# Optimization experiments

Hardware: AMD Instinct MI355X
Metric: run time of the kernel (lower is better)

## Reference

```python
import jax, jax.numpy as jnp
import numpy as np

N_NODES = 50000
N_EDGES = 800000
D = 128
N_GRAPHS = 128
N_CLASSES = 10
BN_EPS = 1e-5


def setup_inputs() -> dict:
    key = jax.random.key(0)
    ks = jax.random.split(key, 8)
    x = jax.random.normal(ks[0], (N_NODES, D), dtype=jnp.float32)
    edge_index = jax.random.randint(ks[1], (2, N_EDGES), 0, N_NODES, dtype=jnp.int64)
    batch = jnp.sort(jax.random.randint(ks[2], (N_NODES,), 0, N_GRAPHS, dtype=jnp.int64))
    s = 1.0 / np.sqrt(D)
    W1a = jax.random.normal(ks[3], (D, D), dtype=jnp.float32) * s
    W1b = jax.random.normal(ks[4], (D, D), dtype=jnp.float32) * s
    W2a = jax.random.normal(ks[5], (D, D), dtype=jnp.float32) * s
    W2b = jax.random.normal(ks[6], (D, D), dtype=jnp.float32) * s
    Wo = jax.random.normal(ks[7], (D, N_CLASSES), dtype=jnp.float32) * s
    z = jnp.zeros((D,), jnp.float32)
    o = jnp.ones((D,), jnp.float32)
    return dict(x=x, edge_index=edge_index, batch=batch,
                W1a=W1a, b1a=z, W1b=W1b, b1b=z, g1=o, be1=z,
                W2a=W2a, b2a=z, W2b=W2b, b2b=z, g2=o, be2=z,
                Wo=Wo, bo=jnp.zeros((N_CLASSES,), jnp.float32))


def _gin_conv(x, edge_index, Wa, ba, Wb, bb):
    # message passing: gather source features, scatter-add to targets (eps=0)
    msgs = x[edge_index[0]]                                   # [E, D]
    agg = jax.ops.segment_sum(msgs, edge_index[1], num_segments=x.shape[0])
    h = agg + x                                               # (1+eps)*x + sum_j x_j
    h = jnp.maximum(h @ Wa + ba, 0.0)                         # Linear -> ReLU
    return h @ Wb + bb                                        # Linear


def _bn_relu(h, gamma, beta):
    # BatchNorm1d (training mode: batch stats, biased var) + ReLU
    mu = jnp.mean(h, axis=0)
    var = jnp.mean(jnp.square(h - mu), axis=0)
    hn = (h - mu) * jax.lax.rsqrt(var + BN_EPS) * gamma + beta
    return jnp.maximum(hn, 0.0)


def reference(x, edge_index, batch,
              W1a, b1a, W1b, b1b, g1, be1,
              W2a, b2a, W2b, b2b, g2, be2,
              Wo, bo):
    h = _gin_conv(x, edge_index, W1a, b1a, W1b, b1b)
    h = _bn_relu(h, g1, be1)
    h = _gin_conv(h, edge_index, W2a, b2a, W2b, b2b)
    h = _bn_relu(h, g2, be2)
    pooled = jax.ops.segment_sum(h, batch, num_segments=N_GRAPHS)  # global_add_pool
    return pooled @ Wo + bo
```

## Files before the change

### kernel.cpp

```cpp
#include <hip/hip_runtime.h>

typedef __attribute__((ext_vector_type(8))) short bf16x8;
typedef __attribute__((ext_vector_type(4))) float f32x4;
typedef __attribute__((ext_vector_type(2))) float f32x2;
typedef __attribute__((ext_vector_type(2))) unsigned u32x2;

#define N_NODES 50000
#define N_EDGES 800000
#define DIM 128
#define N_GRAPHS 128
#define N_CLASSES 10
#define BN_EPS 1e-5f
#define FBLK ((N_NODES + 63) / 64)
#define FGRID (FBLK / 2)
#define NPART (FBLK * 4)
#define RED_NB 64
#define RED_ROWS ((NPART + RED_NB - 1) / RED_NB)

#define NBUCK 196
#define FILL_NB 400
#define FILL_PER (N_EDGES / FILL_NB)
#define BMAX 6144

#define CVT_NB (N_NODES * 64 / 256)
#define PREPW_NB 256

static __device__ __forceinline__ unsigned short f2bf(float f) {
    unsigned u = __float_as_uint(f);
    u += 0x7FFF + ((u >> 16) & 1);
    return (unsigned short)(u >> 16);
}
static __device__ __forceinline__ float bf_lo(unsigned u) { return __uint_as_float(u << 16); }
static __device__ __forceinline__ float bf_hi(unsigned u) { return __uint_as_float(u & 0xffff0000u); }
static __device__ __forceinline__ unsigned packbf(float a, float b) {
    return (unsigned)f2bf(a) | ((unsigned)f2bf(b) << 16);
}

__global__ __launch_bounds__(256) void prep_all(const f32x2* __restrict__ x,
                                                unsigned* __restrict__ xb,
                                                const float* __restrict__ W0,
                                                const float* __restrict__ W1,
                                                const float* __restrict__ W2,
                                                const float* __restrict__ W3,
                                                unsigned short* __restrict__ wf,
                                                const int* __restrict__ batch,
                                                int* __restrict__ gs,
                                                const int* __restrict__ ei,
                                                int* __restrict__ gbcnt) {
    int b = blockIdx.x, tid = threadIdx.x;
    if (b < CVT_NB) {
        int t = b * 256 + tid;
        f32x2 v = x[t];
        xb[t] = packbf(v[0], v[1]);
    } else if (b < CVT_NB + PREPW_NB) {
        int t = (b - CVT_NB) * 256 + tid;
        int m = t >> 14, rem = t & 16383;
        int e = rem & 7, lane = (rem >> 3) & 63, fi = rem >> 9;
        int ks = fi & 3, n = fi >> 2;
        int col = n * 16 + (lane & 15);
        int k = ks * 32 + ((lane >> 4) << 3) + e;
        const float* W = (m == 0) ? W0 : (m == 1) ? W1 : (m == 2) ? W2 : W3;
        wf[t] = f2bf(W[k * DIM + col]);
    } else if (b < CVT_NB + PREPW_NB + FILL_NB) {
        __shared__ int cnt[NBUCK];
        if (tid < NBUCK) cnt[tid] = 0;
        __syncthreads();
        int e0 = (b - CVT_NB - PREPW_NB) * FILL_PER;
        for (int c = tid; c < FILL_PER; c += 256) {
            int dst = ei[N_EDGES + e0 + c];
            atomicAdd(&cnt[dst >> 8], 1);
        }
        __syncthreads();
        if (tid < NBUCK) atomicAdd(&gbcnt[tid], cnt[tid]);
    } else {
        int g = tid;
        if (g > N_GRAPHS) return;
        int lo = 0, hi = N_NODES;
        while (lo < hi) {
            int mid = (lo + hi) >> 1;
            if (batch[mid] < g) lo = mid + 1; else hi = mid;
        }
        gs[g] = lo;
    }
}

__global__ __launch_bounds__(256) void bucket_scan(const int* __restrict__ gbcnt,
                                                   int* __restrict__ boff,
                                                   int* __restrict__ gcur) {
    __shared__ int buf[256];
    int t = threadIdx.x;
    int v = (t < NBUCK) ? gbcnt[t] : 0;
    buf[t] = v;
    __syncthreads();
#pragma unroll
    for (int off = 1; off < 256; off <<= 1) {
        int u = (t >= off) ? buf[t - off] : 0;
        __syncthreads();
        buf[t] += u;
        __syncthreads();
    }
    if (t < NBUCK) { int ex = buf[t] - v; boff[t] = ex; gcur[t] = ex; }
    if (t == 0) boff[NBUCK] = N_EDGES;
}

__global__ __launch_bounds__(256) void bucket_fill(const int* __restrict__ ei,
                                                   int* __restrict__ gcur,
                                                   unsigned* __restrict__ gbuf) {
    __shared__ unsigned ent[FILL_PER];
    __shared__ unsigned srt[FILL_PER];
    __shared__ int cnt[256], c2[256], lofs[256], gbase[256];
    int tid = threadIdx.x;
    int e0 = blockIdx.x * FILL_PER;
    cnt[tid] = 0; c2[tid] = 0;
    __syncthreads();
    for (int i = tid; i < FILL_PER; i += 256) {
        int src = ei[e0 + i];
        int dst = ei[N_EDGES + e0 + i];
        ent[i] = (unsigned)src | ((unsigned)(dst & 255) << 16) | ((unsigned)(dst >> 8) << 24);
        atomicAdd(&cnt[dst >> 8], 1);
    }
    __syncthreads();
    int v = cnt[tid];
    lofs[tid] = v;
    __syncthreads();
#pragma unroll
    for (int off = 1; off < 256; off <<= 1) {
        int u = (tid >= off) ? lofs[tid - off] : 0;
        __syncthreads();
        lofs[tid] += u;
        __syncthreads();
    }
    int excl = lofs[tid] - v;
    lofs[tid] = excl;
    if (tid < NBUCK && v > 0) gbase[tid] = atomicAdd(&gcur[tid], v);
    __syncthreads();
    for (int i = tid; i < FILL_PER; i += 256) {
        unsigned w = ent[i];
        int b = w >> 24;
        int r = atomicAdd(&c2[b], 1);
        srt[lofs[b] + r] = w;
    }
    __syncthreads();
    for (int i = tid; i < FILL_PER; i += 256) {
        unsigned w = srt[i];
        int b = w >> 24;
        gbuf[gbase[b] + (i - lofs[b])] = w;
    }
}

__global__ __launch_bounds__(256) void csr_build(const unsigned* __restrict__ gbuf,
                                                 const int* __restrict__ boff,
                                                 unsigned short* __restrict__ csr16,
                                                 int* __restrict__ row_start) {
    __shared__ unsigned ent[BMAX];
    __shared__ unsigned short csl[BMAX];
    __shared__ int cnt[256], c2[256], offs[256];
    int b = blockIdx.x, t = threadIdx.x;
    int base = boff[b], n = boff[b + 1] - base;
    for (int i = t; i < n; i += 256) ent[i] = gbuf[base + i];
    cnt[t] = 0; c2[t] = 0;
    __syncthreads();
    for (int i = t; i < n; i += 256) atomicAdd(&cnt[(ent[i] >> 16) & 255], 1);
    __syncthreads();
    int v = cnt[t];
    offs[t] = v;
    __syncthreads();
#pragma unroll
    for (int off = 1; off < 256; off <<= 1) {
        int u = (t >= off) ? offs[t - off] : 0;
        __syncthreads();
        offs[t] += u;
        __syncthreads();
    }
    int excl = offs[t] - v;
    int node = b * 256 + t;
    if (node < N_NODES) row_start[node] = base + excl;
    if (b == NBUCK - 1 && t == 0) row_start[N_NODES] = N_EDGES;
    __syncthreads();
    offs[t] = excl;
    __syncthreads();
    for (int i = t; i < n; i += 256) {
        unsigned w = ent[i];
        int d = (w >> 16) & 255;
        int r = atomicAdd(&c2[d], 1);
        csl[offs[d] + r] = (unsigned short)(w & 0xffffu);
    }
    __syncthreads();
    for (int i = t; i < n; i += 256) csr16[base + i] = csl[i];
}

template <bool BN>
__global__ __launch_bounds__(256) void aggregate_bf(const u32x2* __restrict__ F2,
                                                    u32x2* __restrict__ out,
                                                    const int* __restrict__ row_start,
                                                    const unsigned short* __restrict__ csr16,
                                                    const float* __restrict__ scale,
                                                    const float* __restrict__ shift) {
    int wave = threadIdx.x >> 6, lane = threadIdx.x & 63;
    int v = blockIdx.x * 4 + wave;
    if (v >= N_NODES) return;
    int half = lane >> 5;
    int c4 = lane & 31;
    f32x4 sc, sh;
    if (BN) {
        sc = ((const f32x4*)scale)[c4];
        sh = ((const f32x4*)shift)[c4];
    }
    int e0 = row_start[v];
    int n = row_start[v + 1] - e0;
    int myidx = (lane < n) ? (int)csr16[e0 + lane] : 0;
    int n64 = (n < 64) ? n : 64;

    f32x4 a0 = f32x4{0.f, 0.f, 0.f, 0.f};
    f32x4 a1 = f32x4{0.f, 0.f, 0.f, 0.f};
    if (half == 0) {
        u32x2 u = F2[(size_t)v * 32 + c4];
        a0[0] = bf_lo(u[0]); a0[1] = bf_hi(u[0]);
        a0[2] = bf_lo(u[1]); a0[3] = bf_hi(u[1]);
        if (BN) {
#pragma unroll
            for (int k = 0; k < 4; ++k) a0[k] = fmaxf(a0[k] * sc[k] + sh[k], 0.f);
        }
    }

    for (int base = 0; base < n64; base += 8) {
        int j0 = base + half, j1 = j0 + 2, j2 = j0 + 4, j3 = j0 + 6;
        int s0 = __shfl(myidx, j0 & 63, 64);
        int s1 = __shfl(myidx, j1 & 63, 64);
        int s2 = __shfl(myidx, j2 & 63, 64);
        int s3 = __shfl(myidx, j3 & 63, 64);
        u32x2 ua = F2[(size_t)s0 * 32 + c4];
        u32x2 ub = F2[(size_t)s1 * 32 + c4];
        u32x2 uc = F2[(size_t)s2 * 32 + c4];
        u32x2 ud = F2[(size_t)s3 * 32 + c4];
        float p0 = bf_lo(ua[0]), p1 = bf_hi(ua[0]), p2 = bf_lo(ua[1]), p3 = bf_hi(ua[1]);
        float q0 = bf_lo(ub[0]), q1 = bf_hi(ub[0]), q2 = bf_lo(ub[1]), q3 = bf_hi(ub[1]);
        float r0 = bf_lo(uc[0]), r1 = bf_hi(uc[0]), r2 = bf_lo(uc[1]), r3 = bf_hi(uc[1]);
        float t0 = bf_lo(ud[0]), t1 = bf_hi(ud[0]), t2 = bf_lo(ud[1]), t3 = bf_hi(ud[1]);
        if (BN) {
            p0 = fmaxf(p0 * sc[0] + sh[0], 0.f); p1 = fmaxf(p1 * sc[1] + sh[1], 0.f);
            p2 = fmaxf(p2 * sc[2] + sh[2], 0.f); p3 = fmaxf(p3 * sc[3] + sh[3], 0.f);
            q0 = fmaxf(q0 * sc[0] + sh[0], 0.f); q1 = fmaxf(q1 * sc[1] + sh[1], 0.f);
            q2 = fmaxf(q2 * sc[2] + sh[2], 0.f); q3 = fmaxf(q3 * sc[3] + sh[3], 0.f);
            r0 = fmaxf(r0 * sc[0] + sh[0], 0.f); r1 = fmaxf(r1 * sc[1] + sh[1], 0.f);
            r2 = fmaxf(r2 * sc[2] + sh[2], 0.f); r3 = fmaxf(r3 * sc[3] + sh[3], 0.f);
            t0 = fmaxf(t0 * sc[0] + sh[0], 0.f); t1 = fmaxf(t1 * sc[1] + sh[1], 0.f);
            t2 = fmaxf(t2 * sc[2] + sh[2], 0.f); t3 = fmaxf(t3 * sc[3] + sh[3], 0.f);
        }
        if (j0 < n64) { a0[0] += p0; a0[1] += p1; a0[2] += p2; a0[3] += p3; }
        if (j1 < n64) { a0[0] += q0; a0[1] += q1; a0[2] += q2; a0[3] += q3; }
        if (j2 < n64) { a1[0] += r0; a1[1] += r1; a1[2] += r2; a1[3] += r3; }
        if (j3 < n64) { a1[0] += t0; a1[1] += t1; a1[2] += t2; a1[3] += t3; }
    }
    for (int j = 64 + half; j < n; j += 2) {
        int s = csr16[e0 + j];
        u32x2 ua = F2[(size_t)s * 32 + c4];
        float p0 = bf_lo(ua[0]), p1 = bf_hi(ua[0]), p2 = bf_lo(ua[1]), p3 = bf_hi(ua[1]);
        if (BN) {
            p0 = fmaxf(p0 * sc[0] + sh[0], 0.f); p1 = fmaxf(p1 * sc[1] + sh[1], 0.f);
            p2 = fmaxf(p2 * sc[2] + sh[2], 0.f); p3 = fmaxf(p3 * sc[3] + sh[3], 0.f);
        }
        a0[0] += p0; a0[1] += p1; a0[2] += p2; a0[3] += p3;
    }
#pragma unroll
    for (int k = 0; k < 4; ++k) a0[k] += a1[k];
#pragma unroll
    for (int k = 0; k < 4; ++k) a0[k] += __shfl_xor(a0[k], 32, 64);
    if (half == 0) {
        u32x2 w;
        w[0] = packbf(a0[0], a0[1]);
        w[1] = packbf(a0[2], a0[3]);
        out[(size_t)v * 32 + c4] = w;
    }
}

__global__ __launch_bounds__(256, 3) void fused_layer(
        const unsigned short* __restrict__ A,
        const bf16x8* __restrict__ wfA_g,
        const bf16x8* __restrict__ wfB_g,
        const float* __restrict__ bias_a,
        const float* __restrict__ bias_b,
        unsigned short* __restrict__ out,
        float* __restrict__ psum,
        float* __restrict__ psq, int M) {
    __shared__ bf16x8 wfS[2048];
    __shared__ unsigned short mid[8192];

    int tid = threadIdx.x;
    int w = tid >> 6, lane = tid & 63;
    int cl = lane & 15, kq = lane >> 4;

    bf16x8 wa[8], wb[8];
#pragma unroll
    for (int i = 0; i < 8; ++i) wa[i] = wfA_g[i * 256 + tid];
#pragma unroll
    for (int i = 0; i < 8; ++i) wb[i] = wfB_g[i * 256 + tid];

    for (int t = 0; t < 2; ++t) {
        int tile = blockIdx.x + t * FGRID;
        int rblk = tile * 64;

#pragma unroll
        for (int i = 0; i < 8; ++i) wfS[i * 256 + tid] = wa[i];

        int arow = rblk + w * 16 + cl;
        if (arow >= M) arow = M - 1;
        bf16x8 af[4];
        const unsigned short* Ap = A + (size_t)arow * DIM + kq * 8;
#pragma unroll
        for (int ks = 0; ks < 4; ++ks) af[ks] = *(const bf16x8*)(Ap + ks * 32);

        __syncthreads();

        f32x4 acc[8];
#pragma unroll
        for (int n = 0; n < 8; ++n) acc[n] = f32x4{0.f, 0.f, 0.f, 0.f};
#pragma unroll
        for (int n = 0; n < 8; ++n)
#pragma unroll
            for (int ks = 0; ks < 4; ++ks)
                acc[n] = __builtin_amdgcn_mfma_f32_16x16x32_bf16(
                    af[ks], wfS[(n * 4 + ks) * 64 + lane], acc[n], 0, 0, 0);

#pragma unroll
        for (int n = 0; n < 8; ++n) {
            int col = n * 16 + cl;
            float b = bias_a[col];
#pragma unroll
            for (int r = 0; r < 4; ++r) {
                int rl = w * 16 + kq * 4 + r;
                float v = fmaxf(acc[n][r] + b, 0.f);
                mid[(rl * DIM + col) ^ ((rl & 7) << 3)] = f2bf(v);
            }
        }
        __syncthreads();

#pragma unroll
        for (int i = 0; i < 8; ++i) wfS[i * 256 + tid] = wb[i];

        bf16x8 af2[4];
        {
            int rl = w * 16 + cl;
            int sw = (cl & 7) << 3;
#pragma unroll
            for (int ks = 0; ks < 4; ++ks)
                af2[ks] = *(const bf16x8*)(mid + ((rl * DIM + kq * 8 + ks * 32) ^ sw));
        }
        __syncthreads();

        f32x4 acc2[8];
#pragma unroll
        for (int n = 0; n < 8; ++n) acc2[n] = f32x4{0.f, 0.f, 0.f, 0.f};
#pragma unroll
        for (int n = 0; n < 8; ++n)
#pragma unroll
            for (int ks = 0; ks < 4; ++ks)
                acc2[n] = __builtin_amdgcn_mfma_f32_16x16x32_bf16(
                    af2[ks], wfS[(n * 4 + ks) * 64 + lane], acc2[n], 0, 0, 0);

        int prow = tile * 4 + w;
#pragma unroll
        for (int n = 0; n < 8; ++n) {
            int col = n * 16 + cl;
            float b = bias_b[col];
            float s = 0.f, q = 0.f;
#pragma unroll
            for (int r = 0; r < 4; ++r) {
                int rl = w * 16 + kq * 4 + r;
                float v = acc2[n][r] + b;
                if (rblk + rl < M) { s += v; q += v * v; }
                mid[(rl * DIM + col) ^ ((rl & 7) << 3)] = f2bf(v);
            }
            s += __shfl_xor(s, 16, 64);
            s += __shfl_xor(s, 32, 64);
            q += __shfl_xor(q, 16, 64);
            q += __shfl_xor(q, 32, 64);
            if (kq == 0) {
                psum[(size_t)prow * DIM + col] = s;
                psq[(size_t)prow * DIM + col] = q;
            }
        }

        {
            int r4 = lane >> 4, c = lane & 15;
#pragma unroll
            for (int rb = 0; rb < 4; ++rb) {
                int rl = w * 16 + rb * 4 + r4;
                int grow = rblk + rl;
                bf16x8 v = *(const bf16x8*)(mid + ((rl * DIM + c * 8) ^ ((rl & 7) << 3)));
                if (grow < M) *(bf16x8*)(out + (size_t)grow * DIM + c * 8) = v;
            }
        }
        __syncthreads();
    }
}

__global__ __launch_bounds__(256) void reduce_stats(const float* __restrict__ psum,
                                                    const float* __restrict__ psq,
                                                    float* __restrict__ ps2) {
    int b = blockIdx.x, t = threadIdx.x;
    int c = t & 127;
    const float* src = (t < 128) ? psum : psq;
    int r0 = b * RED_ROWS;
    int r1 = min(NPART, r0 + RED_ROWS);
    float acc = 0.f;
    for (int r = r0; r < r1; ++r) acc += src[(size_t)r * DIM + c];
    ps2[(size_t)b * 256 + t] = acc;
}

__global__ __launch_bounds__(256) void bn_finalize(const float* __restrict__ ps2,
                                                   const float* __restrict__ g,
                                                   const float* __restrict__ be,
                                                   float* __restrict__ scale,
                                                   float* __restrict__ shift) {
    __shared__ float sums[128], sqs[128];
    int t = threadIdx.x;
    int c = t & 127;
    float acc = 0.f;
#pragma unroll 4
    for (int r = 0; r < RED_NB; ++r) acc += ps2[(size_t)r * 256 + t];
    if (t < 128) sums[c] = acc; else sqs[c] = acc;
    __syncthreads();
    if (t < 128) {
        const float invN = 1.0f / (float)N_NODES;
        float mu = sums[c] * invN;
        float var = sqs[c] * invN - mu * mu;
        float rs = rsqrtf(var + BN_EPS) * g[c];
        scale[c] = rs;
        shift[c] = be[c] - mu * rs;
    }
}

__global__ __launch_bounds__(256) void bn_pool_final(const unsigned short* __restrict__ h,
                                                     const float* __restrict__ scale,
                                                     const float* __restrict__ shift,
                                                     const int* __restrict__ gs,
                                                     const float* __restrict__ Wo,
                                                     const float* __restrict__ bo,
                                                     float* __restrict__ out) {
    int g = blockIdx.x;
    int t = threadIdx.x;
    int c4 = t & 31;
    int rs = t >> 5;
    int r0 = gs[g], r1 = gs[g + 1];
    f32x4 sc = ((const f32x4*)scale)[c4];
    f32x4 sh = ((const f32x4*)shift)[c4];
    f32x4 acc = f32x4{0.f, 0.f, 0.f, 0.f};
    for (int r = r0 + rs; r < r1; r += 8) {
        u32x2 u = *(const u32x2*)(h + (size_t)r * DIM + c4 * 4);
        float f0 = bf_lo(u[0]), f1 = bf_hi(u[0]), f2 = bf_lo(u[1]), f3 = bf_hi(u[1]);
        acc[0] += fmaxf(f0 * sc[0] + sh[0], 0.f);
        acc[1] += fmaxf(f1 * sc[1] + sh[1], 0.f);
        acc[2] += fmaxf(f2 * sc[2] + sh[2], 0.f);
        acc[3] += fmaxf(f3 * sc[3] + sh[3], 0.f);
    }
    __shared__ f32x4 red[256];
    __shared__ float pf[DIM];
    red[t] = acc;
    __syncthreads();
#pragma unroll
    for (int off = 128; off >= 32; off >>= 1) {
        if (t < off) red[t] += red[t + off];
        __syncthreads();
    }
    if (t < 32) {
        f32x4 r = red[t];
        pf[t * 4 + 0] = r[0]; pf[t * 4 + 1] = r[1];
        pf[t * 4 + 2] = r[2]; pf[t * 4 + 3] = r[3];
    }
    __syncthreads();
    if (t < N_CLASSES) {
        float s = bo[t];
#pragma unroll 8
        for (int k = 0; k < DIM; ++k) s += pf[k] * Wo[k * N_CLASSES + t];
        out[g * N_CLASSES + t] = s;
    }
}

extern "C" void kernel_launch(void* const* d_in, const int* in_sizes, int n_in,
                              void* d_out, int out_size, void* d_ws, size_t ws_size,
                              hipStream_t stream) {
    const float* x   = (const float*)d_in[0];
    const int* ei    = (const int*)d_in[1];
    const int* batch = (const int*)d_in[2];
    const float* W1a = (const float*)d_in[3];
    const float* b1a = (const float*)d_in[4];
    const float* W1b = (const float*)d_in[5];
    const float* b1b = (const float*)d_in[6];
    const float* g1  = (const float*)d_in[7];
    const float* be1 = (const float*)d_in[8];
    const float* W2a = (const float*)d_in[9];
    const float* b2a = (const float*)d_in[10];
    const float* W2b = (const float*)d_in[11];
    const float* b2b = (const float*)d_in[12];
    const float* g2  = (const float*)d_in[13];
    const float* be2 = (const float*)d_in[14];
    const float* Wo  = (const float*)d_in[15];
    const float* bo  = (const float*)d_in[16];

    char* ws = (char*)d_ws;
    const size_t NBH = (size_t)N_NODES * DIM * 2;
    unsigned short* xb   = (unsigned short*)ws;
    unsigned short* aggb = (unsigned short*)(ws + NBH);
    unsigned short* hb   = (unsigned short*)(ws + 2 * NBH);
    unsigned short* wfrag = (unsigned short*)(ws + 3 * NBH);
    float* psum = (float*)(ws + 3 * NBH + 4 * 16384 * 2);
    float* psq  = psum + (size_t)NPART * DIM;
    float* ps2  = psq + (size_t)NPART * DIM;
    float* scale1  = ps2 + RED_NB * 256;
    float* shift1  = scale1 + 128;
    float* scale2  = scale1 + 256;
    float* shift2  = scale1 + 384;
    int* gs        = (int*)(shift2 + 128);
    int* gbcnt     = gs + N_GRAPHS + 1;
    int* boff      = gbcnt + NBUCK;
    int* gcur      = boff + NBUCK + 1;
    int* row_start = gcur + NBUCK;
    unsigned* gbuf = (unsigned*)(row_start + N_NODES + 1);
    unsigned short* csr16 = (unsigned short*)(gbuf + N_EDGES);

    hipMemsetAsync(gbcnt, 0, NBUCK * 4, stream);

    prep_all<<<CVT_NB + PREPW_NB + FILL_NB + 1, 256, 0, stream>>>(
        (const f32x2*)x, (unsigned*)xb, W1a, W1b, W2a, W2b, wfrag, batch, gs, ei, gbcnt);

    bucket_scan<<<1, 256, 0, stream>>>(gbcnt, boff, gcur);
    bucket_fill<<<FILL_NB, 256, 0, stream>>>(ei, gcur, gbuf);
    csr_build<<<NBUCK, 256, 0, stream>>>(gbuf, boff, csr16, row_start);

    const int ablk = (N_NODES + 3) / 4;

    aggregate_bf<false><<<ablk, 256, 0, stream>>>((const u32x2*)xb, (u32x2*)aggb,
                                                  row_start, csr16, nullptr, nullptr);
    fused_layer<<<FGRID, 256, 0, stream>>>(
        aggb, (const bf16x8*)(wfrag + 0 * 16384), (const bf16x8*)(wfrag + 1 * 16384),
        b1a, b1b, hb, psum, psq, N_NODES);
    reduce_stats<<<RED_NB, 256, 0, stream>>>(psum, psq, ps2);
    bn_finalize<<<1, 256, 0, stream>>>(ps2, g1, be1, scale1, shift1);

    aggregate_bf<true><<<ablk, 256, 0, stream>>>((const u32x2*)hb, (u32x2*)aggb,
                                                 row_start, csr16, scale1, shift1);
    fused_layer<<<FGRID, 256, 0, stream>>>(
        aggb, (const bf16x8*)(wfrag + 2 * 16384), (const bf16x8*)(wfrag + 3 * 16384),
        b2a, b2b, hb, psum, psq, N_NODES);
    reduce_stats<<<RED_NB, 256, 0, stream>>>(psum, psq, ps2);
    bn_finalize<<<1, 256, 0, stream>>>(ps2, g2, be2, scale2, shift2);

    bn_pool_final<<<N_GRAPHS, 256, 0, stream>>>(hb, scale2, shift2, gs, Wo, bo,
                                                (float*)d_out);
}
```

Baseline: 220.9 us.

## Fold scan and BN finalize into last-block epilogues; widen aggregation loads to 16B

The bucket scan is merged into prep_all and the BN finalize into the stats reduction. In each case the last block to finish, detected with an atomic counter and thread fences, runs the follow-up work, which removes three small kernel launches and their dependency gaps. Aggregation now uses 16-byte per-lane gathers, with four 16-lane groups each covering one edge row instead of two 32-lane halves. This halves the load instructions per row at the cost of a two-step cross-lane reduction and more registers.

```diff
diff --git a/kernel.cpp b/kernel.cpp
--- a/kernel.cpp
+++ b/kernel.cpp
@@ -4,6 +4,7 @@
 typedef __attribute__((ext_vector_type(4))) float f32x4;
 typedef __attribute__((ext_vector_type(2))) float f32x2;
 typedef __attribute__((ext_vector_type(2))) unsigned u32x2;
+typedef __attribute__((ext_vector_type(4))) unsigned u32x4;
 
 #define N_NODES 50000
 #define N_EDGES 800000
@@ -46,7 +47,10 @@
                                                 const int* __restrict__ batch,
                                                 int* __restrict__ gs,
                                                 const int* __restrict__ ei,
-                                                int* __restrict__ gbcnt) {
+                                                int* __restrict__ gbcnt,
+                                                int* __restrict__ boff,
+                                                int* __restrict__ gcur,
+                                                int* __restrict__ ctr_scan) {
     int b = blockIdx.x, tid = threadIdx.x;
     if (b < CVT_NB) {
         int t = b * 256 + tid;
@@ -63,6 +67,7 @@
         wf[t] = f2bf(W[k * DIM + col]);
     } else if (b < CVT_NB + PREPW_NB + FILL_NB) {
         __shared__ int cnt[NBUCK];
+        __shared__ int done;
         if (tid < NBUCK) cnt[tid] = 0;
         __syncthreads();
         int e0 = (b - CVT_NB - PREPW_NB) * FILL_PER;
@@ -72,6 +77,26 @@
         }
         __syncthreads();
         if (tid < NBUCK) atomicAdd(&gbcnt[tid], cnt[tid]);
+        __threadfence();
+        __syncthreads();
+        if (tid == 0) done = atomicAdd(ctr_scan, 1);
+        __syncthreads();
+        if (done == FILL_NB - 1) {
+            __threadfence();
+            __shared__ int buf[256];
+            int v = (tid < NBUCK) ? gbcnt[tid] : 0;
+            buf[tid] = v;
+            __syncthreads();
+#pragma unroll
+            for (int off = 1; off < 256; off <<= 1) {
+                int u = (tid >= off) ? buf[tid - off] : 0;
+                __syncthreads();
+                buf[tid] += u;
+                __syncthreads();
+            }
+            if (tid < NBUCK) { int ex = buf[tid] - v; boff[tid] = ex; gcur[tid] = ex; }
+            if (tid == 0) boff[NBUCK] = N_EDGES;
+        }
     } else {
         int g = tid;
         if (g > N_GRAPHS) return;
@@ -82,25 +107,6 @@
         }
         gs[g] = lo;
     }
-}
-
-__global__ __launch_bounds__(256) void bucket_scan(const int* __restrict__ gbcnt,
-                                                   int* __restrict__ boff,
-                                                   int* __restrict__ gcur) {
-    __shared__ int buf[256];
-    int t = threadIdx.x;
-    int v = (t < NBUCK) ? gbcnt[t] : 0;
-    buf[t] = v;
-    __syncthreads();
-#pragma unroll
-    for (int off = 1; off < 256; off <<= 1) {
-        int u = (t >= off) ? buf[t - off] : 0;
-        __syncthreads();
-        buf[t] += u;
-        __syncthreads();
-    }
-    if (t < NBUCK) { int ex = buf[t] - v; boff[t] = ex; gcur[t] = ex; }
-    if (t == 0) boff[NBUCK] = N_EDGES;
 }
 
 __global__ __launch_bounds__(256) void bucket_fill(const int* __restrict__ ei,
@@ -190,8 +196,8 @@
 }
 
 template <bool BN>
-__global__ __launch_bounds__(256) void aggregate_bf(const u32x2* __restrict__ F2,
-                                                    u32x2* __restrict__ out,
+__global__ __launch_bounds__(256) void aggregate_bf(const u32x4* __restrict__ F4,
+                                                    u32x4* __restrict__ out,
                                                     const int* __restrict__ row_start,
                                                     const unsigned short* __restrict__ csr16,
                                                     const float* __restrict__ scale,
@@ -199,79 +205,93 @@
     int wave = threadIdx.x >> 6, lane = threadIdx.x & 63;
     int v = blockIdx.x * 4 + wave;
     if (v >= N_NODES) return;
-    int half = lane >> 5;
-    int c4 = lane & 31;
-    f32x4 sc, sh;
+    int q = lane >> 4;
+    int c8 = lane & 15;
+    f32x4 scA, scB, shA, shB;
     if (BN) {
-        sc = ((const f32x4*)scale)[c4];
-        sh = ((const f32x4*)shift)[c4];
+        scA = ((const f32x4*)scale)[c8 * 2];
+        scB = ((const f32x4*)scale)[c8 * 2 + 1];
+        shA = ((const f32x4*)shift)[c8 * 2];
+        shB = ((const f32x4*)shift)[c8 * 2 + 1];
     }
     int e0 = row_start[v];
     int n = row_start[v + 1] - e0;
     int myidx = (lane < n) ? (int)csr16[e0 + lane] : 0;
     int n64 = (n < 64) ? n : 64;
 
-    f32x4 a0 = f32x4{0.f, 0.f, 0.f, 0.f};
-    f32x4 a1 = f32x4{0.f, 0.f, 0.f, 0.f};
-    if (half == 0) {
-        u32x2 u = F2[(size_t)v * 32 + c4];
-        a0[0] = bf_lo(u[0]); a0[1] = bf_hi(u[0]);
-        a0[2] = bf_lo(u[1]); a0[3] = bf_hi(u[1]);
-        if (BN) {
-#pragma unroll
-            for (int k = 0; k < 4; ++k) a0[k] = fmaxf(a0[k] * sc[k] + sh[k], 0.f);
-        }
+    float a[8] = {0.f, 0.f, 0.f, 0.f, 0.f, 0.f, 0.f, 0.f};
+    float bacc[8] = {0.f, 0.f, 0.f, 0.f, 0.f, 0.f, 0.f, 0.f};
+
+#define UNPACK8(U, P)                                                         \
+    P[0] = bf_lo(U[0]); P[1] = bf_hi(U[0]); P[2] = bf_lo(U[1]); P[3] = bf_hi(U[1]); \
+    P[4] = bf_lo(U[2]); P[5] = bf_hi(U[2]); P[6] = bf_lo(U[3]); P[7] = bf_hi(U[3]);
+#define BN8(P)                                                                \
+    if (BN) {                                                                 \
+        P[0] = fmaxf(P[0] * scA[0] + shA[0], 0.f);                            \
+        P[1] = fmaxf(P[1] * scA[1] + shA[1], 0.f);                            \
+        P[2] = fmaxf(P[2] * scA[2] + shA[2], 0.f);                            \
+        P[3] = fmaxf(P[3] * scA[3] + shA[3], 0.f);                            \
+        P[4] = fmaxf(P[4] * scB[0] + shB[0], 0.f);                            \
+        P[5] = fmaxf(P[5] * scB[1] + shB[1], 0.f);                            \
+        P[6] = fmaxf(P[6] * scB[2] + shB[2], 0.f);                            \
+        P[7] = fmaxf(P[7] * scB[3] + shB[3], 0.f);                            \
+    }
+
+    if (q == 0) {
+        u32x4 u = F4[(size_t)v * 16 + c8];
+        float p[8];
+        UNPACK8(u, p)
+        BN8(p)
+#pragma unroll
+        for (int k = 0; k < 8; ++k) a[k] += p[k];
     }
 
     for (int base = 0; base < n64; base += 8) {
-        int j0 = base + half, j1 = j0 + 2, j2 = j0 + 4, j3 = j0 + 6;
+        int j0 = base + q, j1 = base + 4 + q;
         int s0 = __shfl(myidx, j0 & 63, 64);
         int s1 = __shfl(myidx, j1 & 63, 64);
-        int s2 = __shfl(myidx, j2 & 63, 64);
-        int s3 = __shfl(myidx, j3 & 63, 64);
-        u32x2 ua = F2[(size_t)s0 * 32 + c4];
-        u32x2 ub = F2[(size_t)s1 * 32 + c4];
-        u32x2 uc = F2[(size_t)s2 * 32 + c4];
-        u32x2 ud = F2[(size_t)s3 * 32 + c4];
-        float p0 = bf_lo(ua[0]), p1 = bf_hi(ua[0]), p2 = bf_lo(ua[1]), p3 = bf_hi(ua[1]);
-        float q0 = bf_lo(ub[0]), q1 = bf_hi(ub[0]), q2 = bf_lo(ub[1]), q3 = bf_hi(ub[1]);
-        float r0 = bf_lo(uc[0]), r1 = bf_hi(uc[0]), r2 = bf_lo(uc[1]), r3 = bf_hi(uc[1]);
-        float t0 = bf_lo(ud[0]), t1 = bf_hi(ud[0]), t2 = bf_lo(ud[1]), t3 = bf_hi(ud[1]);
-        if (BN) {
-            p0 = fmaxf(p0 * sc[0] + sh[0], 0.f); p1 = fmaxf(p1 * sc[1] + sh[1], 0.f);
-            p2 = fmaxf(p2 * sc[2] + sh[2], 0.f); p3 = fmaxf(p3 * sc[3] + sh[3], 0.f);
-            q0 = fmaxf(q0 * sc[0] + sh[0], 0.f); q1 = fmaxf(q1 * sc[1] + sh[1], 0.f);
-            q2 = fmaxf(q2 * sc[2] + sh[2], 0.f); q3 = fmaxf(q3 * sc[3] + sh[3], 0.f);
-            r0 = fmaxf(r0 * sc[0] + sh[0], 0.f); r1 = fmaxf(r1 * sc[1] + sh[1], 0.f);
-            r2 = fmaxf(r2 * sc[2] + sh[2], 0.f); r3 = fmaxf(r3 * sc[3] + sh[3], 0.f);
-            t0 = fmaxf(t0 * sc[0] + sh[0], 0.f); t1 = fmaxf(t1 * sc[1] + sh[1], 0.f);
-            t2 = fmaxf(t2 * sc[2] + sh[2], 0.f); t3 = fmaxf(t3 * sc[3] + sh[3], 0.f);
-        }
-        if (j0 < n64) { a0[0] += p0; a0[1] += p1; a0[2] += p2; a0[3] += p3; }
-        if (j1 < n64) { a0[0] += q0; a0[1] += q1; a0[2] += q2; a0[3] += q3; }
-        if (j2 < n64) { a1[0] += r0; a1[1] += r1; a1[2] += r2; a1[3] += r3; }
-        if (j3 < n64) { a1[0] += t0; a1[1] += t1; a1[2] += t2; a1[3] += t3; }
-    }
-    for (int j = 64 + half; j < n; j += 2) {
+        u32x4 ua = F4[(size_t)s0 * 16 + c8];
+        u32x4 ub = F4[(size_t)s1 * 16 + c8];
+        float p[8], r[8];
+        UNPACK8(ua, p)
+        UNPACK8(ub, r)
+        BN8(p)
+        BN8(r)
+        if (j0 < n64) {
+#pragma unroll
+            for (int k = 0; k < 8; ++k) a[k] += p[k];
+        }
+        if (j1 < n64) {
+#pragma unroll
+            for (int k = 0; k < 8; ++k) bacc[k] += r[k];
+        }
+    }
+    for (int j = 64 + q; j < n; j += 4) {
         int s = csr16[e0 + j];
-        u32x2 ua = F2[(size_t)s * 32 + c4];
-        float p0 = bf_lo(ua[0]), p1 = bf_hi(ua[0]), p2 = bf_lo(ua[1]), p3 = bf_hi(ua[1]);
-        if (BN) {
-            p0 = fmaxf(p0 * sc[0] + sh[0], 0.f); p1 = fmaxf(p1 * sc[1] + sh[1], 0.f);
-            p2 = fmaxf(p2 * sc[2] + sh[2], 0.f); p3 = fmaxf(p3 * sc[3] + sh[3], 0.f);
-        }
-        a0[0] += p0; a0[1] += p1; a0[2] += p2; a0[3] += p3;
-    }
-#pragma unroll
-    for (int k = 0; k < 4; ++k) a0[k] += a1[k];
-#pragma unroll
-    for (int k = 0; k < 4; ++k) a0[k] += __shfl_xor(a0[k], 32, 64);
-    if (half == 0) {
-        u32x2 w;
-        w[0] = packbf(a0[0], a0[1]);
-        w[1] = packbf(a0[2], a0[3]);
-        out[(size_t)v * 32 + c4] = w;
-    }
+        u32x4 ua = F4[(size_t)s * 16 + c8];
+        float p[8];
+        UNPACK8(ua, p)
+        BN8(p)
+#pragma unroll
+        for (int k = 0; k < 8; ++k) a[k] += p[k];
+    }
+#pragma unroll
+    for (int k = 0; k < 8; ++k) a[k] += bacc[k];
+#pragma unroll
+    for (int k = 0; k < 8; ++k) {
+        a[k] += __shfl_xor(a[k], 16, 64);
+        a[k] += __shfl_xor(a[k], 32, 64);
+    }
+    if (q == 0) {
+        u32x4 w;
+        w[0] = packbf(a[0], a[1]);
+        w[1] = packbf(a[2], a[3]);
+        w[2] = packbf(a[4], a[5]);
+        w[3] = packbf(a[6], a[7]);
+        out[(size_t)v * 16 + c8] = w;
+    }
+#undef UNPACK8
+#undef BN8
 }
 
 __global__ __launch_bounds__(256, 3) void fused_layer(
@@ -395,9 +415,14 @@
     }
 }
 
-__global__ __launch_bounds__(256) void reduce_stats(const float* __restrict__ psum,
-                                                    const float* __restrict__ psq,
-                                                    float* __restrict__ ps2) {
+__global__ __launch_bounds__(256) void stats_all(const float* __restrict__ psum,
+                                                 const float* __restrict__ psq,
+                                                 float* __restrict__ ps2,
+                                                 const float* __restrict__ g,
+                                                 const float* __restrict__ be,
+                                                 float* __restrict__ scale,
+                                                 float* __restrict__ shift,
+                                                 int* __restrict__ ctr) {
     int b = blockIdx.x, t = threadIdx.x;
     int c = t & 127;
     const float* src = (t < 128) ? psum : psq;
@@ -406,28 +431,27 @@
     float acc = 0.f;
     for (int r = r0; r < r1; ++r) acc += src[(size_t)r * DIM + c];
     ps2[(size_t)b * 256 + t] = acc;
-}
-
-__global__ __launch_bounds__(256) void bn_finalize(const float* __restrict__ ps2,
-                                                   const float* __restrict__ g,
-                                                   const float* __restrict__ be,
-                                                   float* __restrict__ scale,
-                                                   float* __restrict__ shift) {
-    __shared__ float sums[128], sqs[128];
-    int t = threadIdx.x;
-    int c = t & 127;
-    float acc = 0.f;
+    __threadfence();
+    __shared__ int done;
+    __syncthreads();
+    if (t == 0) done = atomicAdd(ctr, 1);
+    __syncthreads();
+    if (done == RED_NB - 1) {
+        __threadfence();
+        float a2 = 0.f;
 #pragma unroll 4
-    for (int r = 0; r < RED_NB; ++r) acc += ps2[(size_t)r * 256 + t];
-    if (t < 128) sums[c] = acc; else sqs[c] = acc;
-    __syncthreads();
-    if (t < 128) {
-        const float invN = 1.0f / (float)N_NODES;
-        float mu = sums[c] * invN;
-        float var = sqs[c] * invN - mu * mu;
-        float rs = rsqrtf(var + BN_EPS) * g[c];
-        scale[c] = rs;
-        shift[c] = be[c] - mu * rs;
+        for (int r = 0; r < RED_NB; ++r) a2 += ps2[(size_t)r * 256 + t];
+        __shared__ float sums[128], sqs[128];
+        if (t < 128) sums[c] = a2; else sqs[c] = a2;
+        __syncthreads();
+        if (t < 128) {
+            const float invN = 1.0f / (float)N_NODES;
+            float mu = sums[c] * invN;
+            float var = sqs[c] * invN - mu * mu;
+            float rs = rsqrtf(var + BN_EPS) * g[c];
+            scale[c] = rs;
+            shift[c] = be[c] - mu * rs;
+        }
     }
 }
 
@@ -513,38 +537,39 @@
     float* shift2  = scale1 + 384;
     int* gs        = (int*)(shift2 + 128);
     int* gbcnt     = gs + N_GRAPHS + 1;
-    int* boff      = gbcnt + NBUCK;
+    int* ctrs      = gbcnt + NBUCK;
+    int* boff      = ctrs + 3;
     int* gcur      = boff + NBUCK + 1;
     int* row_start = gcur + NBUCK;
     unsigned* gbuf = (unsigned*)(row_start + N_NODES + 1);
     unsigned short* csr16 = (unsigned short*)(gbuf + N_EDGES);
 
-    hipMemsetAsync(gbcnt, 0, NBUCK * 4, stream);
+    hipMemsetAsync(gbcnt, 0, (NBUCK + 3) * 4, stream);
 
     prep_all<<<CVT_NB + PREPW_NB + FILL_NB + 1, 256, 0, stream>>>(
-        (const f32x2*)x, (unsigned*)xb, W1a, W1b, W2a, W2b, wfrag, batch, gs, ei, gbcnt);
-
-    bucket_scan<<<1, 256, 0, stream>>>(gbcnt, boff, gcur);
+        (const f32x2*)x, (unsigned*)xb, W1a, W1b, W2a, W2b, wfrag, batch, gs, ei,
+        gbcnt, boff, gcur, ctrs + 0);
+
     bucket_fill<<<FILL_NB, 256, 0, stream>>>(ei, gcur, gbuf);
     csr_build<<<NBUCK, 256, 0, stream>>>(gbuf, boff, csr16, row_start);
 
     const int ablk = (N_NODES + 3) / 4;
 
-    aggregate_bf<false><<<ablk, 256, 0, stream>>>((const u32x2*)xb, (u32x2*)aggb,
+    aggregate_bf<false><<<ablk, 256, 0, stream>>>((const u32x4*)xb, (u32x4*)aggb,
                                                   row_start, csr16, nullptr, nullptr);
     fused_layer<<<FGRID, 256, 0, stream>>>(
         aggb, (const bf16x8*)(wfrag + 0 * 16384), (const bf16x8*)(wfrag + 1 * 16384),
         b1a, b1b, hb, psum, psq, N_NODES);
-    reduce_stats<<<RED_NB, 256, 0, stream>>>(psum, psq, ps2);
-    bn_finalize<<<1, 256, 0, stream>>>(ps2, g1, be1, scale1, shift1);
-
-    aggregate_bf<true><<<ablk, 256, 0, stream>>>((const u32x2*)hb, (u32x2*)aggb,
+    stats_all<<<RED_NB, 256, 0, stream>>>(psum, psq, ps2, g1, be1, scale1, shift1,
+                                          ctrs + 1);
+
+    aggregate_bf<true><<<ablk, 256, 0, stream>>>((const u32x4*)hb, (u32x4*)aggb,
                                                  row_start, csr16, scale1, shift1);
     fused_layer<<<FGRID, 256, 0, stream>>>(
         aggb, (const bf16x8*)(wfrag + 2 * 16384), (const bf16x8*)(wfrag + 3 * 16384),
         b2a, b2b, hb, psum, psq, N_NODES);
-    reduce_stats<<<RED_NB, 256, 0, stream>>>(psum, psq, ps2);
-    bn_finalize<<<1, 256, 0, stream>>>(ps2, g2, be2, scale2, shift2);
+    stats_all<<<RED_NB, 256, 0, stream>>>(psum, psq, ps2, g2, be2, scale2, shift2,
+                                          ctrs + 2);
 
     bn_pool_final<<<N_GRAPHS, 256, 0, stream>>>(hb, scale2, shift2, gs, Wo, bo,
                                                 (float*)d_out);
```

New measurement: 242.2 us. 9.7% more time.
